# Kernel optimization log

Hardware: AMD Instinct MI355X
Metric: run time of the kernel (lower is better)

## Reference

```python
import jax, jax.numpy as jnp
import numpy as np

NUM_EMBEDDINGS = 1024
EMBEDDING_DIM = 256
COMMITMENT_COST = 0.25
DECAY = 0.99
EPSILON = 1e-05


def setup_inputs() -> dict:
    key = jax.random.key(0)
    k1, k2, k3 = jax.random.split(key, 3)
    z = jax.random.normal(k1, (32, EMBEDDING_DIM, 32, 32), dtype=jnp.float32)
    codebook = jax.random.normal(k2, (NUM_EMBEDDINGS, EMBEDDING_DIM), dtype=jnp.float32)
    ema_cluster_size = jnp.zeros((NUM_EMBEDDINGS,), dtype=jnp.float32)
    ema_dw = jax.random.normal(k3, (NUM_EMBEDDINGS, EMBEDDING_DIM), dtype=jnp.float32)
    return {"z": z, "codebook": codebook, "ema_cluster_size": ema_cluster_size, "ema_dw": ema_dw}


def reference(z, codebook, ema_cluster_size, ema_dw):
    K, D = codebook.shape
    # (B,C,H,W) -> (B,H,W,C)
    zp = jnp.transpose(z, (0, 2, 3, 1))
    z_flat = zp.reshape(-1, D)  # [N, D]
    N = z_flat.shape[0]

    # squared L2 distances to each code: [N, K]
    distances = (jnp.sum(z_flat ** 2, axis=1, keepdims=True)
                 + jnp.sum(codebook ** 2, axis=1)
                 - 2.0 * z_flat @ codebook.T)
    idx = jnp.argmin(distances, axis=1)  # [N]

    quantized = codebook[idx].reshape(zp.shape)  # [B,H,W,C]

    # training-mode EMA codebook update (one-hot scatter expressed as segment sums)
    counts = jax.ops.segment_sum(jnp.ones((N,), z_flat.dtype), idx, num_segments=K)  # encodings.sum(0)
    dw = jax.ops.segment_sum(z_flat, idx, num_segments=K)                            # encodings.T @ z_flat
    new_cluster_size = ema_cluster_size * DECAY + (1.0 - DECAY) * counts
    new_ema_dw = ema_dw * DECAY + (1.0 - DECAY) * dw
    n = jnp.sum(new_cluster_size)
    cluster_size = (new_cluster_size + EPSILON) / (n + K * EPSILON) * n
    new_codebook = new_ema_dw / cluster_size[:, None]

    commitment_loss = jnp.mean((zp - jax.lax.stop_gradient(quantized)) ** 2)
    loss = COMMITMENT_COST * commitment_loss

    # straight-through estimator
    quantized_st = zp + jax.lax.stop_gradient(quantized - zp)

    avg_probs = counts / N
    perplexity = jnp.exp(-jnp.sum(avg_probs * jnp.log(avg_probs + 1e-10)))

    quantized_out = jnp.transpose(quantized_st, (0, 3, 1, 2))  # back to (B,C,H,W)
    return (quantized_out, loss, perplexity, new_codebook, new_cluster_size, new_ema_dw)
```

## Files before the change

### kernel.cpp

```cpp
#include <hip/hip_runtime.h>
#include <cfloat>
#include <cstdint>

#define B_BATCH 32
#define D_DIM   256
#define HW      1024
#define N_POS   32768
#define K_CODES 1024
#define DECAY_F   0.99f
#define ONE_M_DECAY 0.01f
#define EPS_F   1e-5f

#define OUT_Q    0
#define OUT_LOSS 8388608
#define OUT_PERP 8388609
#define OUT_CB   8388610
#define OUT_NCS  8650754
#define OUT_EDW  8651778


#define WS_COUNTS  0
#define WS_ZNORM   4096
#define WS_BSUM    4100
#define WS_MEMSET  4104
#define WS_CBNORM  4352
#define WS_OFFS    8448
#define WS_CURSOR  12544
#define WS_IDX     16640
#define WS_SORTED  147712
#define WS_CBHI    278784
#define WS_CBLO    803072
#define WS_PART    1327360
#define WS_SCODE   3424512
#define WS_TOTAL   3555584

typedef short s16x8 __attribute__((ext_vector_type(8)));
typedef float f32x4 __attribute__((ext_vector_type(4)));
typedef unsigned long long u64;

__device__ __forceinline__ ushort f2bf_rne(float x) {
    uint u = __float_as_uint(x);
    uint r = (u + 0x7FFF + ((u >> 16) & 1)) >> 16;
    return (ushort)r;
}
__device__ __forceinline__ float bf2f(ushort h) {
    return __uint_as_float(((uint)h) << 16);
}

__device__ __forceinline__ void gload16(const void* g, void* l) {
    __builtin_amdgcn_global_load_lds(
        (const __attribute__((address_space(1))) unsigned*)(uintptr_t)g,
        (__attribute__((address_space(3))) unsigned*)(uintptr_t)l, 16, 0, 0);
}

__global__ __launch_bounds__(256) void prep_ztrans(const float* __restrict__ z,
                                                   const float* __restrict__ cb,
                                                   ushort* __restrict__ zhi,
                                                   ushort* __restrict__ zlo,
                                                   ushort* __restrict__ cbhi,
                                                   ushort* __restrict__ cblo,
                                                   float* __restrict__ cbnorm,
                                                   float* __restrict__ znorm_acc) {
    __shared__ float Zs[32][65];
    __shared__ float red[256];
    const int tid = threadIdx.x;

    if (blockIdx.x >= 512) {
        int wave = tid >> 6;
        int lane = tid & 63;
        int k = (blockIdx.x - 512) * 4 + wave;
        float4 v = *(const float4*)&cb[(size_t)k * D_DIM + lane * 4];
        ushort4 h, l;
        h.x = f2bf_rne(v.x); l.x = f2bf_rne(v.x - bf2f(h.x));
        h.y = f2bf_rne(v.y); l.y = f2bf_rne(v.y - bf2f(h.y));
        h.z = f2bf_rne(v.z); l.z = f2bf_rne(v.z - bf2f(h.z));
        h.w = f2bf_rne(v.w); l.w = f2bf_rne(v.w - bf2f(h.w));
        *(ushort4*)&cbhi[(size_t)k * D_DIM + lane * 4] = h;
        *(ushort4*)&cblo[(size_t)k * D_DIM + lane * 4] = l;
        float s = v.x * v.x + v.y * v.y + v.z * v.z + v.w * v.w;
        #pragma unroll
        for (int off = 32; off >= 1; off >>= 1) s += __shfl_xor(s, off);
        if (lane == 0) cbnorm[k] = s;
        return;
    }

    const int n0  = blockIdx.x * 64;
    const int b   = n0 >> 10;
    const int hw0 = n0 & 1023;
    const float* zb = z + (size_t)b * (D_DIM * HW) + hw0;

    const int zn = tid & 63;
    const int zdb = (tid >> 6) * 8;
    const int n  = tid >> 2;
    const int dq = tid & 3;
    float zsum = 0.f;

    for (int d0 = 0; d0 < D_DIM; d0 += 32) {
        __syncthreads();
        #pragma unroll
        for (int j = 0; j < 8; ++j)
            Zs[zdb + j][zn] = zb[(size_t)(d0 + zdb + j) * HW + zn];
        __syncthreads();
        s16x8 hv, lv;
        #pragma unroll
        for (int j = 0; j < 8; ++j) {
            float f = Zs[dq * 8 + j][n];
            zsum += f * f;
            ushort hb = f2bf_rne(f);
            ushort lb = f2bf_rne(f - bf2f(hb));
            hv[j] = (short)hb;
            lv[j] = (short)lb;
        }
        *(s16x8*)&zhi[(size_t)(n0 + n) * D_DIM + d0 + dq * 8] = hv;
        *(s16x8*)&zlo[(size_t)(n0 + n) * D_DIM + d0 + dq * 8] = lv;
    }
    red[tid] = zsum;
    __syncthreads();
    for (int s2 = 128; s2 >= 1; s2 >>= 1) {
        if (tid < s2) red[tid] += red[tid + s2];
        __syncthreads();
    }
    if (tid == 0) atomicAdd(znorm_acc, red[0]);
}

__global__ __launch_bounds__(512, 2) void argmin_gemm(const ushort* __restrict__ cbhi,
                                                      const ushort* __restrict__ cblo,
                                                      const ushort* __restrict__ zhi,
                                                      const ushort* __restrict__ zlo,
                                                      const float* __restrict__ cbnorm,
                                                      u64* __restrict__ partial) {
    __shared__ __align__(16) ushort lds[73728];

    const int tid  = threadIdx.x;
    const int wave = tid >> 6;
    const int lane = tid & 63;
    const int col  = lane & 15;
    const int lg   = lane >> 4;
    const int wr   = wave >> 1;
    const int wc   = wave & 1;
    const int blk  = blockIdx.x;
    const int mt = (blk >> 3) & 3;
    const int pt = (blk & 7) | ((blk >> 5) << 3);

    const int srow = tid >> 2;
    const int G    = tid & 3;
    const int sg   = (G ^ ((srow >> 1) & 3)) * 16;
    const char* pAh = (const char*)cbhi + (size_t)(mt * 256 + srow) * 512 + sg;
    const char* pAl = (const char*)cblo + (size_t)(mt * 256 + srow) * 512 + sg;
    const char* pBh = (const char*)zhi  + (size_t)(pt * 128 + srow) * 512 + sg;
    const char* pBl = (const char*)zlo  + (size_t)(pt * 128 + srow) * 512 + sg;
    char* const ldsw = (char*)lds + wave * 1024;

    auto stage = [&](int kt, int bsel) {
        char* d = ldsw + bsel * 49152;
        const int kb = kt * 64;
        gload16(pAh + kb,         d);
        gload16(pAh + kb + 65536, d + 8192);
        gload16(pAl + kb,         d + 16384);
        gload16(pAl + kb + 65536, d + 24576);
        gload16(pBh + kb,         d + 32768);
        gload16(pBl + kb,         d + 40960);
    };

    const char* ldsc = (const char*)lds;
    const int swz  = (lg ^ ((col >> 1) & 3)) * 16;
    const int aoff = (wr * 64 + col) * 64 + swz;
    const int boff = (wc * 64 + col) * 64 + swz;

    f32x4 acc[4][4];
    #pragma unroll
    for (int mi = 0; mi < 4; ++mi)
        #pragma unroll
        for (int ni = 0; ni < 4; ++ni) acc[mi][ni] = {0.f, 0.f, 0.f, 0.f};

    stage(0, 0);
    stage(1, 1);

    #pragma unroll
    for (int t = 0; t < 8; ++t) {
        const int cur = t % 3;
        if (t < 7) asm volatile("s_waitcnt vmcnt(6)" ::: "memory");
        else       asm volatile("s_waitcnt vmcnt(0)" ::: "memory");
        __builtin_amdgcn_s_barrier();
        __builtin_amdgcn_sched_barrier(0);
        if (t < 6) stage(t + 2, (t + 2) % 3);

        const int base = cur * 49152;
        s16x8 ah[4], al[4], bh[4], bl[4];
        #pragma unroll
        for (int mi = 0; mi < 4; ++mi) {
            ah[mi] = *(const s16x8*)(ldsc + base + aoff + mi * 1024);
            al[mi] = *(const s16x8*)(ldsc + base + 16384 + aoff + mi * 1024);
        }
        #pragma unroll
        for (int ni = 0; ni < 4; ++ni) {
            bh[ni] = *(const s16x8*)(ldsc + base + 32768 + boff + ni * 1024);
            bl[ni] = *(const s16x8*)(ldsc + base + 40960 + boff + ni * 1024);
        }
        __builtin_amdgcn_s_setprio(1);
        #pragma unroll
        for (int mi = 0; mi < 4; ++mi)
            #pragma unroll
            for (int ni = 0; ni < 4; ++ni) {
                acc[mi][ni] = __builtin_amdgcn_mfma_f32_16x16x32_bf16(ah[mi], bh[ni], acc[mi][ni], 0, 0, 0);
                acc[mi][ni] = __builtin_amdgcn_mfma_f32_16x16x32_bf16(ah[mi], bl[ni], acc[mi][ni], 0, 0, 0);
                acc[mi][ni] = __builtin_amdgcn_mfma_f32_16x16x32_bf16(al[mi], bh[ni], acc[mi][ni], 0, 0, 0);
            }
        __builtin_amdgcn_s_setprio(0);
    }

    const int kbase = mt * 256 + wr * 64;
    u64 best[4] = {~0ull, ~0ull, ~0ull, ~0ull};
    #pragma unroll
    for (int mi = 0; mi < 4; ++mi) {
        float4 cn = *(const float4*)&cbnorm[kbase + mi * 16 + lg * 4];
        const float* cnp = (const float*)&cn;
        #pragma unroll
        for (int ni = 0; ni < 4; ++ni) {
            #pragma unroll
            for (int r = 0; r < 4; ++r) {
                float dist = cnp[r] - 2.f * acc[mi][ni][r];
                uint ub = __float_as_uint(dist);
                ub = ub ^ (uint)(((int)ub >> 31) | 0x80000000);
                u64 key = ((u64)ub << 32) | (uint)(kbase + mi * 16 + lg * 4 + r);
                if (key < best[ni]) best[ni] = key;
            }
        }
    }
    #pragma unroll
    for (int ni = 0; ni < 4; ++ni) {
        u64 o = __shfl_xor(best[ni], 16); if (o < best[ni]) best[ni] = o;
        o = __shfl_xor(best[ni], 32); if (o < best[ni]) best[ni] = o;
    }
    u64* kredp = (u64*)lds;
    if (lane < 16) {
        #pragma unroll
        for (int ni = 0; ni < 4; ++ni)
            kredp[(wc * 64 + ni * 16 + lane) * 4 + wr] = best[ni];
    }
    __syncthreads();
    if (tid < 128) {
        u64 a = kredp[tid * 4 + 0];
        u64 b = kredp[tid * 4 + 1]; if (b < a) a = b;
        b = kredp[tid * 4 + 2]; if (b < a) a = b;
        b = kredp[tid * 4 + 3]; if (b < a) a = b;
        partial[(size_t)(pt * 128 + tid) * 4 + mt] = a;
    }
}

__global__ __launch_bounds__(256) void combine_kernel(const u64* __restrict__ partial,
                                                      int* __restrict__ idx,
                                                      float* __restrict__ counts,
                                                      float* __restrict__ bsum_acc) {
    __shared__ int hist[1024];
    __shared__ float red[256];
    const int tid = threadIdx.x;
    for (int j = tid; j < 1024; j += 256) hist[j] = 0;
    __syncthreads();
    int n = blockIdx.x * 256 + tid;
    const u64* p = partial + (size_t)n * 4;
    u64 m = p[0];
    #pragma unroll
    for (int j = 1; j < 4; ++j) { u64 v = p[j]; if (v < m) m = v; }
    int k = (int)(m & 1023u);
    idx[n] = k;
    atomicAdd(&hist[k], 1);
    uint ub = (uint)(m >> 32);
    uint u = (ub & 0x80000000u) ? (ub ^ 0x80000000u) : ~ub;
    red[tid] = __uint_as_float(u);
    __syncthreads();
    for (int s2 = 128; s2 >= 1; s2 >>= 1) {
        if (tid < s2) red[tid] += red[tid + s2];
        __syncthreads();
    }
    if (tid == 0) atomicAdd(bsum_acc, red[0]);
    for (int j = tid; j < 1024; j += 256) {
        int c = hist[j];
        if (c) atomicAdd(&counts[j], (float)c);
    }
}

__global__ __launch_bounds__(1024) void small_kernel(const float* __restrict__ ema_cs,
                                                     const float* __restrict__ counts,
                                                     const float* __restrict__ znorm,
                                                     const float* __restrict__ bsum,
                                                     float* __restrict__ out_ncs,
                                                     float* __restrict__ out_perp,
                                                     float* __restrict__ out_loss,
                                                     float* __restrict__ ntot_ws,
                                                     int* __restrict__ offsets,
                                                     int* __restrict__ cursor) {
    __shared__ float s1[1024];
    __shared__ float s2[1024];
    __shared__ int   s3[1024];
    int k = threadIdx.x;
    float cnt = counts[k];
    float ncs = ema_cs[k] * DECAY_F + ONE_M_DECAY * cnt;
    out_ncs[k] = ncs;
    float p = cnt / (float)N_POS;
    s1[k] = ncs;
    s2[k] = p * logf(p + 1e-10f);
    int c = (int)cnt;
    s3[k] = c;
    __syncthreads();
    for (int off = 1; off < 1024; off <<= 1) {
        int v = (k >= off) ? s3[k - off] : 0;
        __syncthreads();
        s3[k] += v;
        __syncthreads();
    }
    int excl = s3[k] - c;
    offsets[k] = excl;
    cursor[k] = excl;
    for (int st = 512; st >= 1; st >>= 1) {
        if (k < st) { s1[k] += s1[k + st]; s2[k] += s2[k + st]; }
        __syncthreads();
    }
    if (k == 0) {
        ntot_ws[0] = s1[0];
        out_perp[0] = expf(-s2[0]);
        out_loss[0] = 0.25f * (znorm[0] + bsum[0]) / 8388608.0f;
    }
}

__global__ __launch_bounds__(256) void scatter_kernel(const int* __restrict__ idx,
                                                      int* __restrict__ cursor,
                                                      int* __restrict__ sorted,
                                                      int* __restrict__ scode,
                                                      float* __restrict__ dw_zero) {
    __shared__ int hist[1024];
    __shared__ int base_s[1024];
    const int tid = threadIdx.x;
    {
        float4 z4 = {0.f, 0.f, 0.f, 0.f};
        size_t e = ((size_t)blockIdx.x * 256 + tid) * 8;
        *(float4*)&dw_zero[e] = z4;
        *(float4*)&dw_zero[e + 4] = z4;
    }
    for (int j = tid; j < 1024; j += 256) hist[j] = 0;
    __syncthreads();
    int n = blockIdx.x * 256 + tid;
    int k = idx[n];
    atomicAdd(&hist[k], 1);
    __syncthreads();
    for (int j = tid; j < 1024; j += 256) {
        int c = hist[j];
        if (c) base_s[j] = atomicAdd(&cursor[j], c);
        hist[j] = 0;
    }
    __syncthreads();
    int rank = atomicAdd(&hist[k], 1);
    int pos = base_s[k] + rank;
    sorted[pos] = n;
    scode[pos] = k;
}

#define DW_CHUNK 64
__global__ __launch_bounds__(256) void dw_chunk_kernel(const ushort* __restrict__ zhi,
                                                       const ushort* __restrict__ zlo,
                                                       const int* __restrict__ sorted,
                                                       const int* __restrict__ scode,
                                                       const int* __restrict__ offsets,
                                                       const float* __restrict__ counts,
                                                       float* __restrict__ dw) {
    __shared__ int sid[DW_CHUNK];
    __shared__ int sk[DW_CHUNK];
    const int tid = threadIdx.x;
    const int p0 = blockIdx.x * DW_CHUNK;
    if (tid < DW_CHUNK) {
        sid[tid] = sorted[p0 + tid];
        sk[tid]  = scode[p0 + tid];
    }
    __syncthreads();
    float acc = 0.f;
    int runstart = 0;
    #pragma unroll 4
    for (int i = 0; i < DW_CHUNK; ++i) {
        int id = sid[i];
        float zv = bf2f(zhi[(size_t)id * D_DIM + tid]) + bf2f(zlo[(size_t)id * D_DIM + tid]);
        acc += zv;
        bool end = (i == DW_CHUNK - 1) || (sk[i + 1] != sk[i]);
        if (end) {
            int k = sk[i];
            int off = offsets[k];
            int cnt = (int)counts[k];
            if (p0 + runstart == off && p0 + i == off + cnt - 1)
                dw[(size_t)k * D_DIM + tid] = acc;
            else
                atomicAdd(&dw[(size_t)k * D_DIM + tid], acc);
            acc = 0.f;
            runstart = i + 1;
        }
    }
}

__global__ __launch_bounds__(256) void fuse_lite(const float* __restrict__ cb,
                                                 const int* __restrict__ idx,
                                                 float* __restrict__ outq) {
    __shared__ float Qs[32][65];
    __shared__ int kidx[64];
    const int tid = threadIdx.x;
    const int n0  = blockIdx.x * 64;
    const int b   = n0 >> 10;
    const int hw0 = n0 & 1023;
    float* ob = outq + (size_t)b * (D_DIM * HW) + hw0;

    if (tid < 64) kidx[tid] = idx[n0 + tid];

    for (int d0 = 0; d0 < D_DIM; d0 += 32) {
        __syncthreads();
        #pragma unroll
        for (int h = 0; h < 2; ++h) {
            int s  = tid + 256 * h;
            int n  = s >> 3;
            int dq = s & 7;
            int k  = kidx[n];
            float4 q = *(const float4*)&cb[(size_t)k * D_DIM + d0 + dq * 4];
            Qs[dq * 4 + 0][n] = q.x;
            Qs[dq * 4 + 1][n] = q.y;
            Qs[dq * 4 + 2][n] = q.z;
            Qs[dq * 4 + 3][n] = q.w;
        }
        __syncthreads();
        #pragma unroll
        for (int j = 0; j < 8; ++j) {
            int v = tid + 256 * j;
            int d = v >> 6;
            int n = v & 63;
            ob[(size_t)(d0 + d) * HW + n] = Qs[d][n];
        }
    }
}

__global__ __launch_bounds__(256) void finalize_rows(const float* __restrict__ ema_dw,
                                                     const float* __restrict__ out_ncs,
                                                     const float* __restrict__ ntot_ws,
                                                     float* __restrict__ out_edw,
                                                     float* __restrict__ out_cb) {
    int k = blockIdx.x;
    int d = threadIdx.x;
    float ncs = out_ncs[k];
    float nt = ntot_ws[0];
    float csz = (ncs + EPS_F) / (nt + (float)K_CODES * EPS_F) * nt;
    size_t e = (size_t)k * D_DIM + d;
    float ed = ema_dw[e] * DECAY_F + ONE_M_DECAY * out_edw[e];
    out_edw[e] = ed;
    out_cb[e] = ed / csz;
}

extern "C" void kernel_launch(void* const* d_in, const int* in_sizes, int n_in,
                              void* d_out, int out_size, void* d_ws, size_t ws_size,
                              hipStream_t stream) {
    const float* z       = (const float*)d_in[0];
    const float* cb      = (const float*)d_in[1];
    const float* ema_cs  = (const float*)d_in[2];
    const float* ema_dw  = (const float*)d_in[3];
    float* out = (float*)d_out;

    char* ws = (char*)d_ws;
    float* ws_counts = (float*)(ws + WS_COUNTS);
    float* ws_znorm  = (float*)(ws + WS_ZNORM);
    float* ws_bsum   = (float*)(ws + WS_BSUM);
    float* ws_cbnorm = (float*)(ws + WS_CBNORM);
    int*   ws_offs   = (int*)(ws + WS_OFFS);
    int*   ws_cursor = (int*)(ws + WS_CURSOR);
    int*   ws_idx    = (int*)(ws + WS_IDX);
    int*   ws_sorted = (int*)(ws + WS_SORTED);
    ushort* ws_cbhi  = (ushort*)(ws + WS_CBHI);
    ushort* ws_cblo  = (ushort*)(ws + WS_CBLO);
    u64*   ws_part   = (u64*)(ws + WS_PART);
    int*   ws_scode  = (int*)(ws + WS_SCODE);

    ushort* zhi = (ushort*)out;
    ushort* zlo = zhi + 8388608;

    hipMemsetAsync(d_ws, 0, WS_MEMSET, stream);

    prep_ztrans<<<768, 256, 0, stream>>>(z, cb, zhi, zlo, ws_cbhi, ws_cblo,
                                         ws_cbnorm, ws_znorm);
    argmin_gemm<<<1024, 512, 0, stream>>>(ws_cbhi, ws_cblo, zhi, zlo, ws_cbnorm, ws_part);
    combine_kernel<<<N_POS / 256, 256, 0, stream>>>(ws_part, ws_idx, ws_counts, ws_bsum);
    small_kernel<<<1, 1024, 0, stream>>>(ema_cs, ws_counts, ws_znorm, ws_bsum,
                                         out + OUT_NCS, out + OUT_PERP, out + OUT_LOSS,
                                         (float*)(ws + WS_ZNORM) + 1024, ws_offs, ws_cursor);
    scatter_kernel<<<N_POS / 256, 256, 0, stream>>>(ws_idx, ws_cursor, ws_sorted,
                                                    ws_scode, out + OUT_EDW);
    dw_chunk_kernel<<<N_POS / DW_CHUNK, 256, 0, stream>>>(zhi, zlo, ws_sorted, ws_scode,
                                                          ws_offs, ws_counts, out + OUT_EDW);
    fuse_lite<<<N_POS / 64, 256, 0, stream>>>(cb, ws_idx, out + OUT_Q);
    finalize_rows<<<K_CODES, 256, 0, stream>>>(ema_dw, out + OUT_NCS,
                                               (float*)(ws + WS_ZNORM) + 1024,
                                               out + OUT_EDW, out + OUT_CB);
}
```

Measured before the change: 209.6 us.

## Interleave LDS reads, prefetch and MFMA in argmin GEMM; fuse tail kernels

The GEMM main loop is split into four MFMA quadrants. LDS fragment reads and the next-stage global prefetches (now split into two halves) are interleaved between them, so that memory traffic overlaps with matrix-core work and register pressure drops. Separately, the quantized-output gather and the EMA finalize kernels are merged into one launch using block-index ranges, which saves one kernel launch and lets the two independent tails run concurrently. The two parts of the merged kernel never touch the same data, so the merge is safe, though the vmcnt waits must still line up with the new load ordering.

```diff
diff --git a/kernel.cpp b/kernel.cpp
--- a/kernel.cpp
+++ b/kernel.cpp
@@ -151,14 +151,18 @@
     const char* pBl = (const char*)zlo  + (size_t)(pt * 128 + srow) * 512 + sg;
     char* const ldsw = (char*)lds + wave * 1024;
 
-    auto stage = [&](int kt, int bsel) {
+    auto stage_a = [&](int kt, int bsel) {
         char* d = ldsw + bsel * 49152;
         const int kb = kt * 64;
         gload16(pAh + kb,         d);
         gload16(pAh + kb + 65536, d + 8192);
+        gload16(pBh + kb,         d + 32768);
+    };
+    auto stage_b = [&](int kt, int bsel) {
+        char* d = ldsw + bsel * 49152;
+        const int kb = kt * 64;
         gload16(pAl + kb,         d + 16384);
         gload16(pAl + kb + 65536, d + 24576);
-        gload16(pBh + kb,         d + 32768);
         gload16(pBl + kb,         d + 40960);
     };
 
@@ -173,8 +177,13 @@
         #pragma unroll
         for (int ni = 0; ni < 4; ++ni) acc[mi][ni] = {0.f, 0.f, 0.f, 0.f};
 
-    stage(0, 0);
-    stage(1, 1);
+    stage_a(0, 0); stage_b(0, 0);
+    stage_a(1, 1); stage_b(1, 1);
+
+#define MM3(mi, ni)                                                                                  \
+    acc[mi][ni] = __builtin_amdgcn_mfma_f32_16x16x32_bf16(ah[mi], bh[ni], acc[mi][ni], 0, 0, 0);     \
+    acc[mi][ni] = __builtin_amdgcn_mfma_f32_16x16x32_bf16(ah[mi], bl[ni], acc[mi][ni], 0, 0, 0);     \
+    acc[mi][ni] = __builtin_amdgcn_mfma_f32_16x16x32_bf16(al[mi], bh[ni], acc[mi][ni], 0, 0, 0);
 
     #pragma unroll
     for (int t = 0; t < 8; ++t) {
@@ -183,31 +192,45 @@
         else       asm volatile("s_waitcnt vmcnt(0)" ::: "memory");
         __builtin_amdgcn_s_barrier();
         __builtin_amdgcn_sched_barrier(0);
-        if (t < 6) stage(t + 2, (t + 2) % 3);
-
-        const int base = cur * 49152;
+
+        const char* bp = ldsc + cur * 49152;
         s16x8 ah[4], al[4], bh[4], bl[4];
-        #pragma unroll
-        for (int mi = 0; mi < 4; ++mi) {
-            ah[mi] = *(const s16x8*)(ldsc + base + aoff + mi * 1024);
-            al[mi] = *(const s16x8*)(ldsc + base + 16384 + aoff + mi * 1024);
-        }
-        #pragma unroll
-        for (int ni = 0; ni < 4; ++ni) {
-            bh[ni] = *(const s16x8*)(ldsc + base + 32768 + boff + ni * 1024);
-            bl[ni] = *(const s16x8*)(ldsc + base + 40960 + boff + ni * 1024);
-        }
+
+        ah[0] = *(const s16x8*)(bp + aoff);
+        al[0] = *(const s16x8*)(bp + 16384 + aoff);
+        ah[1] = *(const s16x8*)(bp + aoff + 1024);
+        al[1] = *(const s16x8*)(bp + 16384 + aoff + 1024);
+        bh[0] = *(const s16x8*)(bp + 32768 + boff);
+        bl[0] = *(const s16x8*)(bp + 40960 + boff);
+        bh[1] = *(const s16x8*)(bp + 32768 + boff + 1024);
+        bl[1] = *(const s16x8*)(bp + 40960 + boff + 1024);
+        if (t < 6) stage_a(t + 2, (t + 2) % 3);
         __builtin_amdgcn_s_setprio(1);
-        #pragma unroll
-        for (int mi = 0; mi < 4; ++mi)
-            #pragma unroll
-            for (int ni = 0; ni < 4; ++ni) {
-                acc[mi][ni] = __builtin_amdgcn_mfma_f32_16x16x32_bf16(ah[mi], bh[ni], acc[mi][ni], 0, 0, 0);
-                acc[mi][ni] = __builtin_amdgcn_mfma_f32_16x16x32_bf16(ah[mi], bl[ni], acc[mi][ni], 0, 0, 0);
-                acc[mi][ni] = __builtin_amdgcn_mfma_f32_16x16x32_bf16(al[mi], bh[ni], acc[mi][ni], 0, 0, 0);
-            }
+        MM3(0, 0) MM3(0, 1) MM3(1, 0) MM3(1, 1)
         __builtin_amdgcn_s_setprio(0);
-    }
+
+        bh[2] = *(const s16x8*)(bp + 32768 + boff + 2048);
+        bl[2] = *(const s16x8*)(bp + 40960 + boff + 2048);
+        bh[3] = *(const s16x8*)(bp + 32768 + boff + 3072);
+        bl[3] = *(const s16x8*)(bp + 40960 + boff + 3072);
+        if (t < 6) stage_b(t + 2, (t + 2) % 3);
+        __builtin_amdgcn_s_setprio(1);
+        MM3(0, 2) MM3(0, 3) MM3(1, 2) MM3(1, 3)
+        __builtin_amdgcn_s_setprio(0);
+
+        ah[2] = *(const s16x8*)(bp + aoff + 2048);
+        al[2] = *(const s16x8*)(bp + 16384 + aoff + 2048);
+        ah[3] = *(const s16x8*)(bp + aoff + 3072);
+        al[3] = *(const s16x8*)(bp + 16384 + aoff + 3072);
+        __builtin_amdgcn_s_setprio(1);
+        MM3(2, 2) MM3(2, 3) MM3(3, 2) MM3(3, 3)
+        __builtin_amdgcn_s_setprio(0);
+
+        __builtin_amdgcn_s_setprio(1);
+        MM3(2, 0) MM3(2, 1) MM3(3, 0) MM3(3, 1)
+        __builtin_amdgcn_s_setprio(0);
+    }
+#undef MM3
 
     const int kbase = mt * 256 + wr * 64;
     u64 best[4] = {~0ull, ~0ull, ~0ull, ~0ull};
@@ -394,12 +417,30 @@
     }
 }
 
-__global__ __launch_bounds__(256) void fuse_lite(const float* __restrict__ cb,
-                                                 const int* __restrict__ idx,
-                                                 float* __restrict__ outq) {
+__global__ __launch_bounds__(256) void tail_fused(const float* __restrict__ cb,
+                                                  const int* __restrict__ idx,
+                                                  float* __restrict__ outq,
+                                                  const float* __restrict__ ema_dw,
+                                                  const float* __restrict__ out_ncs,
+                                                  const float* __restrict__ ntot_ws,
+                                                  float* __restrict__ out_edw,
+                                                  float* __restrict__ out_cb) {
+    const int tid = threadIdx.x;
+    if (blockIdx.x >= 512) {
+        int k = blockIdx.x - 512;
+        int d = tid;
+        float ncs = out_ncs[k];
+        float nt = ntot_ws[0];
+        float csz = (ncs + EPS_F) / (nt + (float)K_CODES * EPS_F) * nt;
+        size_t e = (size_t)k * D_DIM + d;
+        float ed = ema_dw[e] * DECAY_F + ONE_M_DECAY * out_edw[e];
+        out_edw[e] = ed;
+        out_cb[e] = ed / csz;
+        return;
+    }
+
     __shared__ float Qs[32][65];
     __shared__ int kidx[64];
-    const int tid = threadIdx.x;
     const int n0  = blockIdx.x * 64;
     const int b   = n0 >> 10;
     const int hw0 = n0 & 1023;
@@ -430,22 +471,6 @@
             ob[(size_t)(d0 + d) * HW + n] = Qs[d][n];
         }
     }
-}
-
-__global__ __launch_bounds__(256) void finalize_rows(const float* __restrict__ ema_dw,
-                                                     const float* __restrict__ out_ncs,
-                                                     const float* __restrict__ ntot_ws,
-                                                     float* __restrict__ out_edw,
-                                                     float* __restrict__ out_cb) {
-    int k = blockIdx.x;
-    int d = threadIdx.x;
-    float ncs = out_ncs[k];
-    float nt = ntot_ws[0];
-    float csz = (ncs + EPS_F) / (nt + (float)K_CODES * EPS_F) * nt;
-    size_t e = (size_t)k * D_DIM + d;
-    float ed = ema_dw[e] * DECAY_F + ONE_M_DECAY * out_edw[e];
-    out_edw[e] = ed;
-    out_cb[e] = ed / csz;
 }
 
 extern "C" void kernel_launch(void* const* d_in, const int* in_sizes, int n_in,
@@ -487,8 +512,7 @@
                                                     ws_scode, out + OUT_EDW);
     dw_chunk_kernel<<<N_POS / DW_CHUNK, 256, 0, stream>>>(zhi, zlo, ws_sorted, ws_scode,
                                                           ws_offs, ws_counts, out + OUT_EDW);
-    fuse_lite<<<N_POS / 64, 256, 0, stream>>>(cb, ws_idx, out + OUT_Q);
-    finalize_rows<<<K_CODES, 256, 0, stream>>>(ema_dw, out + OUT_NCS,
-                                               (float*)(ws + WS_ZNORM) + 1024,
-                                               out + OUT_EDW, out + OUT_CB);
-}
+    tail_fused<<<1536, 256, 0, stream>>>(cb, ws_idx, out + OUT_Q, ema_dw, out + OUT_NCS,
+                                         (float*)(ws + WS_ZNORM) + 1024,
+                                         out + OUT_EDW, out + OUT_CB);
+}
```

Result: faster. 204.8 us (-2.3%).
